# Performance work log

Measured on AMD Instinct MI355X. Metric: run time of the kernel, lower is better.

Reference implementation:

```python
import jax, jax.numpy as jnp
import numpy as np

N_NODES = 50000
N_EDGES = 800000
IN_DIM = 256
HID = 256
OUT = 2


def setup_inputs() -> dict:
    key = jax.random.key(0)
    ks = jax.random.split(key, 12)
    x = jax.random.normal(ks[0], (N_NODES, IN_DIM), dtype=jnp.float32)
    edge_index = jax.random.randint(ks[1], (2, N_EDGES), 0, N_NODES, dtype=jnp.int64)
    s = lambda fan_in: 1.0 / np.sqrt(fan_in)
    return {
        "x": x,
        "edge_index": edge_index,
        # SAGEConv 1: lin_l (neighbors, with bias), lin_r (root, no bias)
        "W1l": jax.random.normal(ks[2], (IN_DIM, HID), dtype=jnp.float32) * s(IN_DIM),
        "b1l": jnp.zeros((HID,), dtype=jnp.float32),
        "W1r": jax.random.normal(ks[3], (IN_DIM, HID), dtype=jnp.float32) * s(IN_DIM),
        # SAGEConv 2
        "W2l": jax.random.normal(ks[4], (HID, HID), dtype=jnp.float32) * s(HID),
        "b2l": jnp.zeros((HID,), dtype=jnp.float32),
        "W2r": jax.random.normal(ks[5], (HID, HID), dtype=jnp.float32) * s(HID),
        # edge MLP: Linear(2H -> H), ReLU, Linear(H -> OUT)
        "Wm1": jax.random.normal(ks[6], (2 * HID, HID), dtype=jnp.float32) * s(2 * HID),
        "bm1": jnp.zeros((HID,), dtype=jnp.float32),
        "Wm2": jax.random.normal(ks[7], (HID, OUT), dtype=jnp.float32) * s(HID),
        "bm2": jnp.zeros((OUT,), dtype=jnp.float32),
    }


def _sage_conv(x, src, dst, Wl, bl, Wr):
    # mean-aggregate source features at destination nodes (PyG SAGEConv, aggr='mean')
    n = x.shape[0]
    msg_sum = jax.ops.segment_sum(x[src], dst, num_segments=n)      # [N, D]
    deg = jax.ops.segment_sum(jnp.ones((src.shape[0],), x.dtype), dst, num_segments=n)
    agg = msg_sum / jnp.maximum(deg, 1.0)[:, None]
    return agg @ Wl + bl + x @ Wr


def reference(x, edge_index, W1l, b1l, W1r, W2l, b2l, W2r, Wm1, bm1, Wm2, bm2):
    src, dst = edge_index[0], edge_index[1]
    h = jax.nn.relu(_sage_conv(x, src, dst, W1l, b1l, W1r))
    h = jax.nn.relu(_sage_conv(h, src, dst, W2l, b2l, W2r))
    edge_reps = jnp.concatenate([h[src], h[dst]], axis=1)           # [E, 2H]
    hidden = jax.nn.relu(edge_reps @ Wm1 + bm1)
    logits = hidden @ Wm2 + bm2                                     # [E, OUT]
    return logits
```

## Files before the change

kernel.cpp:

```cpp
#include <hip/hip_runtime.h>

#define IN_DIM 256
#define HID 256
#define SCAN_CHUNK 512
#define PADW 264

typedef unsigned short ushort_t;
typedef __attribute__((ext_vector_type(8))) short short8;
typedef __attribute__((ext_vector_type(4))) float floatx4;

__device__ __forceinline__ float b2f(ushort_t h) {
    union { unsigned int u; float f; } c; c.u = ((unsigned int)h) << 16; return c.f;
}
__device__ __forceinline__ ushort_t f2b(float f) {
    union { float f; unsigned int u; } c; c.f = f;
    unsigned int u = c.u;
    unsigned int r = (u + 0x7fffu + ((u >> 16) & 1u)) >> 16;
    return (ushort_t)r;
}

__global__ void k_count_deg(const int* __restrict__ dst, int* __restrict__ deg, int E) {
    int e = blockIdx.x * blockDim.x + threadIdx.x;
    if (e < E) atomicAdd(&deg[dst[e]], 1);
}

__global__ __launch_bounds__(64) void k_chunk_sum(const int* __restrict__ deg,
                                                  int* __restrict__ partials, int N) {
    int lane = threadIdx.x;
    int base = blockIdx.x * SCAN_CHUNK + lane * 8;
    int s = 0;
#pragma unroll
    for (int i = 0; i < 8; ++i) s += (base + i < N) ? deg[base + i] : 0;
#pragma unroll
    for (int off = 32; off > 0; off >>= 1) s += __shfl_down(s, off, 64);
    if (lane == 0) partials[blockIdx.x] = s;
}

__global__ __launch_bounds__(64) void k_scan_partials(int* __restrict__ partials, int nb) {
    int lane = threadIdx.x;
    int run = 0;
    for (int base = 0; base < nb; base += 64) {
        int v = (base + lane < nb) ? partials[base + lane] : 0;
        int s = v;
#pragma unroll
        for (int off = 1; off < 64; off <<= 1) {
            int t = __shfl_up(s, off, 64);
            if (lane >= off) s += t;
        }
        if (base + lane < nb) partials[base + lane] = run + s - v;
        run += __shfl(s, 63, 64);
    }
}

__global__ __launch_bounds__(64) void k_scan_chunks(const int* __restrict__ deg,
                                                    const int* __restrict__ partials,
                                                    int* __restrict__ row_start,
                                                    int* __restrict__ cursor, int N) {
    int lane = threadIdx.x;
    int base = blockIdx.x * SCAN_CHUNK + lane * 8;
    int v[8]; int lsum = 0;
#pragma unroll
    for (int i = 0; i < 8; ++i) { v[i] = (base + i < N) ? deg[base + i] : 0; lsum += v[i]; }
    int pre = lsum;
#pragma unroll
    for (int off = 1; off < 64; off <<= 1) {
        int t = __shfl_up(pre, off, 64);
        if (lane >= off) pre += t;
    }
    pre -= lsum;
    int run = partials[blockIdx.x] + pre;
#pragma unroll
    for (int i = 0; i < 8; ++i) {
        if (base + i < N) { row_start[base + i] = run; cursor[base + i] = run; }
        run += v[i];
    }
}

__global__ void k_bucket(const int* __restrict__ src, const int* __restrict__ dst,
                         int* __restrict__ cursor, int2* __restrict__ csr, int E) {
    int e = blockIdx.x * blockDim.x + threadIdx.x;
    if (e < E) {
        int pos = atomicAdd(&cursor[dst[e]], 1);
        csr[pos] = make_int2(src[e], e);
    }
}

__global__ __launch_bounds__(256) void k_cast(const float* __restrict__ x,
                                              ushort_t* __restrict__ xb, int n4) {
    int i = blockIdx.x * blockDim.x + threadIdx.x;
    if (i >= n4) return;
    float4 v = ((const float4*)x)[i];
    ushort4 o;
    o.x = f2b(v.x); o.y = f2b(v.y); o.z = f2b(v.z); o.w = f2b(v.w);
    ((ushort4*)xb)[i] = o;
}

__global__ __launch_bounds__(64) void k_wprep(const float* __restrict__ Wsrc,
                                              ushort_t* __restrict__ WF,
                                              int nbTot, int nb0) {
    int lane = threadIdx.x;
    int kb = blockIdx.x >> 4, nbL = blockIdx.x & 15;
    int k = kb * 32 + (lane >> 4) * 8;
    int n = nbL * 16 + (lane & 15);
    size_t dstb = (size_t)(kb * nbTot + nb0 + nbL) * 512 + lane * 8;
#pragma unroll
    for (int j = 0; j < 8; ++j) {
        WF[dstb + j] = f2b(Wsrc[(size_t)(k + j) * 256 + n]);
    }
}

__global__ __launch_bounds__(256) void k_gather(const ushort_t* __restrict__ X,
                                                const int2* __restrict__ csr,
                                                const int* __restrict__ row_start,
                                                const int* __restrict__ deg,
                                                ushort_t* __restrict__ agg, int N) {
    int lane = threadIdx.x & 63;
    int node = blockIdx.x * 4 + (threadIdx.x >> 6);
    if (node >= N) return;
    int quad = lane >> 4, l16 = lane & 15;
    int start = row_start[node];
    int cnt = deg[node];
    const int2* sp = csr + start;
    float acc[16] = {};
    for (int b = 0; b < cnt; b += 64) {
        int nb = min(64, cnt - b);
        int sidx = (lane < nb) ? sp[b + lane].x : 0;

        int jA = (quad < nb) ? quad : 0;
        int jB = (4 + quad < nb) ? 4 + quad : 0;
        int sA = __shfl(sidx, jA, 64);
        int sB = __shfl(sidx, jB, 64);
        const ushort_t* rA = X + (size_t)sA * HID + l16 * 16;
        const ushort_t* rB = X + (size_t)sB * HID + l16 * 16;
        short8 a0 = *(const short8*)(rA);
        short8 a1 = *(const short8*)(rA + 8);
        short8 b0 = *(const short8*)(rB);
        short8 b1 = *(const short8*)(rB + 8);

        for (int j8 = 0; j8 < nb; j8 += 8) {
            bool vA = (j8 + quad) < nb, vB = (j8 + 4 + quad) < nb;
            short8 na0 = a0, na1 = a1, nb0 = b0, nb1 = b1;
            int j1 = j8 + 8;
            if (j1 < nb) {
                int cA = (j1 + quad < nb) ? j1 + quad : 0;
                int cB = (j1 + 4 + quad < nb) ? j1 + 4 + quad : 0;
                int zA = __shfl(sidx, cA, 64);
                int zB = __shfl(sidx, cB, 64);
                const ushort_t* qA = X + (size_t)zA * HID + l16 * 16;
                const ushort_t* qB = X + (size_t)zB * HID + l16 * 16;
                na0 = *(const short8*)(qA);
                na1 = *(const short8*)(qA + 8);
                nb0 = *(const short8*)(qB);
                nb1 = *(const short8*)(qB + 8);
            }
            if (vA) {
#pragma unroll
                for (int i = 0; i < 8; ++i) {
                    acc[i]     += b2f((ushort_t)a0[i]);
                    acc[8 + i] += b2f((ushort_t)a1[i]);
                }
            }
            if (vB) {
#pragma unroll
                for (int i = 0; i < 8; ++i) {
                    acc[i]     += b2f((ushort_t)b0[i]);
                    acc[8 + i] += b2f((ushort_t)b1[i]);
                }
            }
            a0 = na0; a1 = na1; b0 = nb0; b1 = nb1;
        }
    }
#pragma unroll
    for (int i = 0; i < 16; ++i) {
        acc[i] += __shfl_down(acc[i], 32, 64);
        acc[i] += __shfl_down(acc[i], 16, 64);
    }
    if (quad == 0) {
        float sc = 1.0f / (float)max(cnt, 1);
        short8 o0, o1;
#pragma unroll
        for (int i = 0; i < 8; ++i) {
            o0[i] = (short)f2b(acc[i] * sc);
            o1[i] = (short)f2b(acc[8 + i] * sc);
        }
        ushort_t* op = agg + (size_t)node * HID + l16 * 16;
        *(short8*)(op) = o0;
        *(short8*)(op + 8) = o1;
    }
}

__global__ __launch_bounds__(512) void k_mfma(const ushort_t* __restrict__ A1,
                                              const ushort_t* __restrict__ WF1,
                                              const ushort_t* __restrict__ A2,
                                              const ushort_t* __restrict__ WF2,
                                              const float* __restrict__ bias, int relu,
                                              int M, int nbTot,
                                              ushort_t* __restrict__ C,
                                              ushort_t* __restrict__ C2) {
    __shared__ ushort_t As[64 * PADW];
    const int tid = threadIdx.x;
    const int lane = tid & 63;
    const int w = tid >> 6;
    const int wm = w >> 2, wn = w & 3;
    const int quad = lane >> 4, l16 = lane & 15;
    const int m0 = blockIdx.y * 64;
    const int n0 = blockIdx.x * 256;
    const int nbBase = (n0 >> 4) + wn * 4;

    floatx4 acc[2][4] = {};

    for (int op = 0; op < 2; ++op) {
        const ushort_t* A = op ? A2 : A1;
        const ushort_t* WF = op ? WF2 : WF1;
        if (A == nullptr) continue;
        if (op) __syncthreads();
#pragma unroll
        for (int i = 0; i < 4; ++i) {
            int c = i * 512 + tid;
            int row = c >> 5, col = c & 31;
            int arow = m0 + row; if (arow >= M) arow = M - 1;
            *(uint4*)&As[row * PADW + col * 8] =
                *(const uint4*)(A + (size_t)arow * 256 + col * 8);
        }
        __syncthreads();

        const ushort_t* a0p = &As[(wm * 32 + l16) * PADW + quad * 8];
        const ushort_t* a1p = a0p + 16 * PADW;
        const ushort_t* wp = WF + (size_t)nbBase * 512 + lane * 8;
#pragma unroll
        for (int kb = 0; kb < 8; ++kb) {
            short8 a0 = *(const short8*)(a0p + kb * 32);
            short8 a1 = *(const short8*)(a1p + kb * 32);
            const ushort_t* wkb = wp + (size_t)kb * nbTot * 512;
#pragma unroll
            for (int nj = 0; nj < 4; ++nj) {
                short8 bj = *(const short8*)(wkb + nj * 512);
                acc[0][nj] = __builtin_amdgcn_mfma_f32_16x16x32_bf16(a0, bj, acc[0][nj], 0, 0, 0);
                acc[1][nj] = __builtin_amdgcn_mfma_f32_16x16x32_bf16(a1, bj, acc[1][nj], 0, 0, 0);
            }
        }
    }

#pragma unroll
    for (int mi = 0; mi < 2; ++mi) {
#pragma unroll
        for (int nj = 0; nj < 4; ++nj) {
            int col = n0 + wn * 64 + nj * 16 + l16;
            float b = bias ? bias[col] : 0.f;
            int rbase = m0 + wm * 32 + mi * 16 + quad * 4;
            ushort_t* dstp = C;
            int c = col;
            if (C2 && col >= 256) { dstp = C2; c = col - 256; }
#pragma unroll
            for (int reg = 0; reg < 4; ++reg) {
                int r = rbase + reg;
                if (r >= M) continue;
                float v = acc[mi][nj][reg] + b;
                if (relu) v = fmaxf(v, 0.f);
                dstp[(size_t)r * 256 + c] = f2b(v);
            }
        }
    }
}

__global__ __launch_bounds__(256) void k_edge(const ushort_t* __restrict__ P,
                                              const ushort_t* __restrict__ Q,
                                              const int2* __restrict__ csr,
                                              const int* __restrict__ row_start,
                                              const int* __restrict__ deg,
                                              const float* __restrict__ bm1,
                                              const float* __restrict__ Wm2,
                                              const float* __restrict__ bm2,
                                              float* __restrict__ out, int N, int stride) {
    int lane = threadIdx.x & 63;
    int wid = blockIdx.x * 4 + (threadIdx.x >> 6);
    int half = lane >> 5, l32 = lane & 31;

    float w0[8], w1[8], bb[8];
    const float* bp = bm1 + l32 * 8;
    const float2* wp = (const float2*)Wm2 + l32 * 8;
#pragma unroll
    for (int i = 0; i < 8; ++i) {
        float2 wv = wp[i];
        w0[i] = wv.x; w1[i] = wv.y;
        bb[i] = bp[i];
    }
    float bo0 = bm2[0], bo1 = bm2[1];

    for (int node = wid; node < N; node += stride) {
        int start = row_start[node];
        int cnt = deg[node];
        if (cnt == 0) continue;

        short8 qv = *(const short8*)(Q + (size_t)node * HID + l32 * 8);
        float qb[8];
#pragma unroll
        for (int i = 0; i < 8; ++i) qb[i] = b2f((ushort_t)qv[i]) + bb[i];

        const int2* sp = csr + start;
        for (int b = 0; b < cnt; b += 64) {
            int nb = min(64, cnt - b);
            int2 se = (lane < nb) ? sp[b + lane] : make_int2(0, 0);

            int iA = (half < nb) ? half : 0;
            int iB = (2 + half < nb) ? 2 + half : 0;
            int iC = (4 + half < nb) ? 4 + half : 0;
            int iD = (6 + half < nb) ? 6 + half : 0;
            int sA = __shfl(se.x, iA, 64);
            int sB = __shfl(se.x, iB, 64);
            int sC = __shfl(se.x, iC, 64);
            int sD = __shfl(se.x, iD, 64);
            short8 pA = *(const short8*)(P + (size_t)sA * HID + l32 * 8);
            short8 pB = *(const short8*)(P + (size_t)sB * HID + l32 * 8);
            short8 pC = *(const short8*)(P + (size_t)sC * HID + l32 * 8);
            short8 pD = *(const short8*)(P + (size_t)sD * HID + l32 * 8);

            for (int j0 = 0; j0 < nb; j0 += 8) {
                bool vA = j0 + half < nb, vB = j0 + 2 + half < nb;
                bool vC = j0 + 4 + half < nb, vD = j0 + 6 + half < nb;

                int kA = iA, kB = iB, kC = iC, kD = iD;
                short8 nA = pA, nB = pB, nC = pC, nD = pD;
                int j1 = j0 + 8;
                if (j1 < nb) {
                    kA = (j1 + half < nb) ? j1 + half : 0;
                    kB = (j1 + 2 + half < nb) ? j1 + 2 + half : 0;
                    kC = (j1 + 4 + half < nb) ? j1 + 4 + half : 0;
                    kD = (j1 + 6 + half < nb) ? j1 + 6 + half : 0;
                    int zA = __shfl(se.x, kA, 64);
                    int zB = __shfl(se.x, kB, 64);
                    int zC = __shfl(se.x, kC, 64);
                    int zD = __shfl(se.x, kD, 64);
                    nA = *(const short8*)(P + (size_t)zA * HID + l32 * 8);
                    nB = *(const short8*)(P + (size_t)zB * HID + l32 * 8);
                    nC = *(const short8*)(P + (size_t)zC * HID + l32 * 8);
                    nD = *(const short8*)(P + (size_t)zD * HID + l32 * 8);
                }

                float aA0 = 0.f, aA1 = 0.f, aB0 = 0.f, aB1 = 0.f;
                float aC0 = 0.f, aC1 = 0.f, aD0 = 0.f, aD1 = 0.f;
#pragma unroll
                for (int i = 0; i < 8; ++i) {
                    float hA = fmaxf(b2f((ushort_t)pA[i]) + qb[i], 0.f);
                    float hB = fmaxf(b2f((ushort_t)pB[i]) + qb[i], 0.f);
                    float hC = fmaxf(b2f((ushort_t)pC[i]) + qb[i], 0.f);
                    float hD = fmaxf(b2f((ushort_t)pD[i]) + qb[i], 0.f);
                    aA0 += hA * w0[i]; aA1 += hA * w1[i];
                    aB0 += hB * w0[i]; aB1 += hB * w1[i];
                    aC0 += hC * w0[i]; aC1 += hC * w1[i];
                    aD0 += hD * w0[i]; aD1 += hD * w1[i];
                }
#pragma unroll
                for (int off = 16; off > 0; off >>= 1) {
                    aA0 += __shfl_down(aA0, off, 32);
                    aA1 += __shfl_down(aA1, off, 32);
                    aB0 += __shfl_down(aB0, off, 32);
                    aB1 += __shfl_down(aB1, off, 32);
                    aC0 += __shfl_down(aC0, off, 32);
                    aC1 += __shfl_down(aC1, off, 32);
                    aD0 += __shfl_down(aD0, off, 32);
                    aD1 += __shfl_down(aD1, off, 32);
                }
                int eA = __shfl(se.y, iA, 64);
                int eB = __shfl(se.y, iB, 64);
                int eC = __shfl(se.y, iC, 64);
                int eD = __shfl(se.y, iD, 64);
                if (l32 == 0) {
                    if (vA) { float2 o; o.x = aA0 + bo0; o.y = aA1 + bo1; ((float2*)out)[eA] = o; }
                    if (vB) { float2 o; o.x = aB0 + bo0; o.y = aB1 + bo1; ((float2*)out)[eB] = o; }
                    if (vC) { float2 o; o.x = aC0 + bo0; o.y = aC1 + bo1; ((float2*)out)[eC] = o; }
                    if (vD) { float2 o; o.x = aD0 + bo0; o.y = aD1 + bo1; ((float2*)out)[eD] = o; }
                }
                pA = nA; pB = nB; pC = nC; pD = nD;
                iA = kA; iB = kB; iC = kC; iD = kD;
            }
        }
    }
}

extern "C" void kernel_launch(void* const* d_in, const int* in_sizes, int n_in,
                              void* d_out, int out_size, void* d_ws, size_t ws_size,
                              hipStream_t stream) {
    const float* x   = (const float*)d_in[0];
    const int*   ei  = (const int*)d_in[1];
    const float* W1l = (const float*)d_in[2];
    const float* b1l = (const float*)d_in[3];
    const float* W1r = (const float*)d_in[4];
    const float* W2l = (const float*)d_in[5];
    const float* b2l = (const float*)d_in[6];
    const float* W2r = (const float*)d_in[7];
    const float* Wm1 = (const float*)d_in[8];
    const float* bm1 = (const float*)d_in[9];
    const float* Wm2 = (const float*)d_in[10];
    const float* bm2 = (const float*)d_in[11];

    const int N = in_sizes[0] / IN_DIM;
    const int E = in_sizes[1] / 2;
    const int* src = ei;
    const int* dst = ei + E;
    const int NB = (N + SCAN_CHUNK - 1) / SCAN_CHUNK;

    char* ws = (char*)d_ws;
    size_t off = 0;
    auto alloc = [&](size_t bytes) { void* p = ws + off; off = (off + bytes + 255) & ~(size_t)255; return p; };
    int* deg       = (int*)alloc((size_t)N * 4);
    int* row_start = (int*)alloc((size_t)N * 4);
    int* cursor    = (int*)alloc((size_t)N * 4);
    int* partials  = (int*)alloc((size_t)(NB + 1) * 4);
    int2* csr      = (int2*)alloc((size_t)E * 8);
    size_t matB = (size_t)N * HID * sizeof(ushort_t);
    ushort_t* xb   = (ushort_t*)alloc(matB);
    ushort_t* aggB = (ushort_t*)alloc(matB);
    ushort_t* h1b  = (ushort_t*)alloc(matB);
    ushort_t* h2b  = (ushort_t*)alloc(matB);
    ushort_t* Pb   = (ushort_t*)alloc(matB);
    ushort_t* Qb   = (ushort_t*)alloc(matB);
    size_t wfB  = (size_t)8 * 16 * 512 * sizeof(ushort_t);
    ushort_t* WF1l = (ushort_t*)alloc(wfB);
    ushort_t* WF1r = (ushort_t*)alloc(wfB);
    ushort_t* WF2l = (ushort_t*)alloc(wfB);
    ushort_t* WF2r = (ushort_t*)alloc(wfB);
    ushort_t* WFm  = (ushort_t*)alloc(wfB * 2);
    float* out = (float*)d_out;

    int nwg = (N + 3) / 4;
    int mrows = (N + 63) / 64;

    hipMemsetAsync(deg, 0, (size_t)N * 4, stream);
    k_count_deg<<<(E + 255) / 256, 256, 0, stream>>>(dst, deg, E);
    k_chunk_sum<<<NB, 64, 0, stream>>>(deg, partials, N);
    k_scan_partials<<<1, 64, 0, stream>>>(partials, NB);
    k_scan_chunks<<<NB, 64, 0, stream>>>(deg, partials, row_start, cursor, N);
    k_bucket<<<(E + 255) / 256, 256, 0, stream>>>(src, dst, cursor, csr, E);

    k_cast<<<(N * HID / 4 + 255) / 256, 256, 0, stream>>>(x, xb, N * HID / 4);
    k_wprep<<<128, 64, 0, stream>>>(W1l, WF1l, 16, 0);
    k_wprep<<<128, 64, 0, stream>>>(W1r, WF1r, 16, 0);
    k_wprep<<<128, 64, 0, stream>>>(W2l, WF2l, 16, 0);
    k_wprep<<<128, 64, 0, stream>>>(W2r, WF2r, 16, 0);
    k_wprep<<<128, 64, 0, stream>>>(Wm1, WFm, 32, 0);
    k_wprep<<<128, 64, 0, stream>>>(Wm1 + (size_t)256 * 256, WFm, 32, 16);

    k_gather<<<nwg, 256, 0, stream>>>(xb, csr, row_start, deg, aggB, N);
    k_mfma<<<dim3(1, mrows), 512, 0, stream>>>(aggB, WF1l, xb, WF1r, b1l, 1, N, 16, h1b, nullptr);

    k_gather<<<nwg, 256, 0, stream>>>(h1b, csr, row_start, deg, aggB, N);
    k_mfma<<<dim3(1, mrows), 512, 0, stream>>>(aggB, WF2l, h1b, WF2r, b2l, 1, N, 16, h2b, nullptr);

    k_mfma<<<dim3(2, mrows), 512, 0, stream>>>(h2b, WFm, nullptr, nullptr, nullptr, 0, N, 32, Pb, Qb);

    const int EB = 2048;
    k_edge<<<EB, 256, 0, stream>>>(Pb, Qb, csr, row_start, deg, bm1, Wm2, bm2, out, N, EB * 4);
}
```

Baseline: 551.8 us.

## Partition edge MLP by source-node slice for P cache locality

Builds a second CSR keyed by (source slice, destination), so the edge kernel processes edges grouped into eight source-node ranges, with blocks assigned to slices. Each slice's P rows (about 3 MB of bf16) should then stay resident in cache during the random gathers. The cost is extra atomics, a larger scan, extra CSR/dst buffers, and a per-edge Q gather in place of the per-node Q reuse. Prefetch double-buffering of the P loads is also dropped.

```diff
diff --git a/kernel.cpp b/kernel.cpp
--- a/kernel.cpp
+++ b/kernel.cpp
@@ -4,6 +4,7 @@
 #define HID 256
 #define SCAN_CHUNK 512
 #define PADW 264
+#define NSLICE 8
 
 typedef unsigned short ushort_t;
 typedef __attribute__((ext_vector_type(8))) short short8;
@@ -19,9 +20,16 @@
     return (ushort_t)r;
 }
 
-__global__ void k_count_deg(const int* __restrict__ dst, int* __restrict__ deg, int E) {
+__global__ void k_count_both(const int* __restrict__ src, const int* __restrict__ dst,
+                             int* __restrict__ deg, int* __restrict__ deg2,
+                             int E, int N, float invS) {
     int e = blockIdx.x * blockDim.x + threadIdx.x;
-    if (e < E) atomicAdd(&deg[dst[e]], 1);
+    if (e < E) {
+        int d = dst[e];
+        atomicAdd(&deg[d], 1);
+        int sl = min((int)((float)src[e] * invS), NSLICE - 1);
+        atomicAdd(&deg2[sl * N + d], 1);
+    }
 }
 
 __global__ __launch_bounds__(64) void k_chunk_sum(const int* __restrict__ deg,
@@ -76,12 +84,20 @@
     }
 }
 
-__global__ void k_bucket(const int* __restrict__ src, const int* __restrict__ dst,
-                         int* __restrict__ cursor, int2* __restrict__ csr, int E) {
+__global__ void k_bucket_both(const int* __restrict__ src, const int* __restrict__ dst,
+                              int* __restrict__ cursor, int2* __restrict__ csr,
+                              int* __restrict__ cursor2, int2* __restrict__ csr2,
+                              int* __restrict__ dst2,
+                              int E, int N, float invS) {
     int e = blockIdx.x * blockDim.x + threadIdx.x;
     if (e < E) {
-        int pos = atomicAdd(&cursor[dst[e]], 1);
-        csr[pos] = make_int2(src[e], e);
+        int s = src[e], d = dst[e];
+        int pos = atomicAdd(&cursor[d], 1);
+        csr[pos] = make_int2(s, e);
+        int sl = min((int)((float)s * invS), NSLICE - 1);
+        int pos2 = atomicAdd(&cursor2[sl * N + d], 1);
+        csr2[pos2] = make_int2(s, e);
+        dst2[pos2] = d;
     }
 }
 
@@ -265,114 +281,95 @@
 
 __global__ __launch_bounds__(256) void k_edge(const ushort_t* __restrict__ P,
                                               const ushort_t* __restrict__ Q,
-                                              const int2* __restrict__ csr,
-                                              const int* __restrict__ row_start,
-                                              const int* __restrict__ deg,
+                                              const int2* __restrict__ csr2,
+                                              const int* __restrict__ dst2,
+                                              const int* __restrict__ rs2,
                                               const float* __restrict__ bm1,
                                               const float* __restrict__ Wm2,
                                               const float* __restrict__ bm2,
-                                              float* __restrict__ out, int N, int stride) {
+                                              float* __restrict__ out, int N, int E) {
     int lane = threadIdx.x & 63;
-    int wid = blockIdx.x * 4 + (threadIdx.x >> 6);
     int half = lane >> 5, l32 = lane & 31;
+    int slice = blockIdx.x & (NSLICE - 1);
+    int wv = (blockIdx.x >> 3) * 4 + (threadIdx.x >> 6);
+    int wstride = (gridDim.x >> 3) * 4;
 
     float w0[8], w1[8], bb[8];
     const float* bp = bm1 + l32 * 8;
     const float2* wp = (const float2*)Wm2 + l32 * 8;
 #pragma unroll
     for (int i = 0; i < 8; ++i) {
-        float2 wv = wp[i];
-        w0[i] = wv.x; w1[i] = wv.y;
+        float2 wv2 = wp[i];
+        w0[i] = wv2.x; w1[i] = wv2.y;
         bb[i] = bp[i];
     }
     float bo0 = bm2[0], bo1 = bm2[1];
 
-    for (int node = wid; node < N; node += stride) {
-        int start = row_start[node];
-        int cnt = deg[node];
-        if (cnt == 0) continue;
-
-        short8 qv = *(const short8*)(Q + (size_t)node * HID + l32 * 8);
-        float qb[8];
-#pragma unroll
-        for (int i = 0; i < 8; ++i) qb[i] = b2f((ushort_t)qv[i]) + bb[i];
-
-        const int2* sp = csr + start;
-        for (int b = 0; b < cnt; b += 64) {
-            int nb = min(64, cnt - b);
-            int2 se = (lane < nb) ? sp[b + lane] : make_int2(0, 0);
-
-            int iA = (half < nb) ? half : 0;
-            int iB = (2 + half < nb) ? 2 + half : 0;
-            int iC = (4 + half < nb) ? 4 + half : 0;
-            int iD = (6 + half < nb) ? 6 + half : 0;
+    int e0 = rs2[slice * N];
+    int e1 = (slice == NSLICE - 1) ? E : rs2[(slice + 1) * N];
+
+    for (int base = e0 + wv * 64; base < e1; base += wstride * 64) {
+        int nb = min(64, e1 - base);
+        int2 se = (lane < nb) ? csr2[base + lane] : make_int2(0, 0);
+        int dd = (lane < nb) ? dst2[base + lane] : 0;
+
+        for (int j0 = 0; j0 < nb; j0 += 8) {
+            bool vA = j0 + half < nb, vB = j0 + 2 + half < nb;
+            bool vC = j0 + 4 + half < nb, vD = j0 + 6 + half < nb;
+            int iA = vA ? j0 + half : 0;
+            int iB = vB ? j0 + 2 + half : 0;
+            int iC = vC ? j0 + 4 + half : 0;
+            int iD = vD ? j0 + 6 + half : 0;
             int sA = __shfl(se.x, iA, 64);
             int sB = __shfl(se.x, iB, 64);
             int sC = __shfl(se.x, iC, 64);
             int sD = __shfl(se.x, iD, 64);
+            int dA = __shfl(dd, iA, 64);
+            int dB = __shfl(dd, iB, 64);
+            int dC = __shfl(dd, iC, 64);
+            int dD = __shfl(dd, iD, 64);
             short8 pA = *(const short8*)(P + (size_t)sA * HID + l32 * 8);
             short8 pB = *(const short8*)(P + (size_t)sB * HID + l32 * 8);
             short8 pC = *(const short8*)(P + (size_t)sC * HID + l32 * 8);
             short8 pD = *(const short8*)(P + (size_t)sD * HID + l32 * 8);
-
-            for (int j0 = 0; j0 < nb; j0 += 8) {
-                bool vA = j0 + half < nb, vB = j0 + 2 + half < nb;
-                bool vC = j0 + 4 + half < nb, vD = j0 + 6 + half < nb;
-
-                int kA = iA, kB = iB, kC = iC, kD = iD;
-                short8 nA = pA, nB = pB, nC = pC, nD = pD;
-                int j1 = j0 + 8;
-                if (j1 < nb) {
-                    kA = (j1 + half < nb) ? j1 + half : 0;
-                    kB = (j1 + 2 + half < nb) ? j1 + 2 + half : 0;
-                    kC = (j1 + 4 + half < nb) ? j1 + 4 + half : 0;
-                    kD = (j1 + 6 + half < nb) ? j1 + 6 + half : 0;
-                    int zA = __shfl(se.x, kA, 64);
-                    int zB = __shfl(se.x, kB, 64);
-                    int zC = __shfl(se.x, kC, 64);
-                    int zD = __shfl(se.x, kD, 64);
-                    nA = *(const short8*)(P + (size_t)zA * HID + l32 * 8);
-                    nB = *(const short8*)(P + (size_t)zB * HID + l32 * 8);
-                    nC = *(const short8*)(P + (size_t)zC * HID + l32 * 8);
-                    nD = *(const short8*)(P + (size_t)zD * HID + l32 * 8);
-                }
-
-                float aA0 = 0.f, aA1 = 0.f, aB0 = 0.f, aB1 = 0.f;
-                float aC0 = 0.f, aC1 = 0.f, aD0 = 0.f, aD1 = 0.f;
-#pragma unroll
-                for (int i = 0; i < 8; ++i) {
-                    float hA = fmaxf(b2f((ushort_t)pA[i]) + qb[i], 0.f);
-                    float hB = fmaxf(b2f((ushort_t)pB[i]) + qb[i], 0.f);
-                    float hC = fmaxf(b2f((ushort_t)pC[i]) + qb[i], 0.f);
-                    float hD = fmaxf(b2f((ushort_t)pD[i]) + qb[i], 0.f);
-                    aA0 += hA * w0[i]; aA1 += hA * w1[i];
-                    aB0 += hB * w0[i]; aB1 += hB * w1[i];
-                    aC0 += hC * w0[i]; aC1 += hC * w1[i];
-                    aD0 += hD * w0[i]; aD1 += hD * w1[i];
-                }
-#pragma unroll
-                for (int off = 16; off > 0; off >>= 1) {
-                    aA0 += __shfl_down(aA0, off, 32);
-                    aA1 += __shfl_down(aA1, off, 32);
-                    aB0 += __shfl_down(aB0, off, 32);
-                    aB1 += __shfl_down(aB1, off, 32);
-                    aC0 += __shfl_down(aC0, off, 32);
-                    aC1 += __shfl_down(aC1, off, 32);
-                    aD0 += __shfl_down(aD0, off, 32);
-                    aD1 += __shfl_down(aD1, off, 32);
-                }
-                int eA = __shfl(se.y, iA, 64);
-                int eB = __shfl(se.y, iB, 64);
-                int eC = __shfl(se.y, iC, 64);
-                int eD = __shfl(se.y, iD, 64);
-                if (l32 == 0) {
-                    if (vA) { float2 o; o.x = aA0 + bo0; o.y = aA1 + bo1; ((float2*)out)[eA] = o; }
-                    if (vB) { float2 o; o.x = aB0 + bo0; o.y = aB1 + bo1; ((float2*)out)[eB] = o; }
-                    if (vC) { float2 o; o.x = aC0 + bo0; o.y = aC1 + bo1; ((float2*)out)[eC] = o; }
-                    if (vD) { float2 o; o.x = aD0 + bo0; o.y = aD1 + bo1; ((float2*)out)[eD] = o; }
-                }
-                pA = nA; pB = nB; pC = nC; pD = nD;
-                iA = kA; iB = kB; iC = kC; iD = kD;
+            short8 qA = *(const short8*)(Q + (size_t)dA * HID + l32 * 8);
+            short8 qB = *(const short8*)(Q + (size_t)dB * HID + l32 * 8);
+            short8 qC = *(const short8*)(Q + (size_t)dC * HID + l32 * 8);
+            short8 qD = *(const short8*)(Q + (size_t)dD * HID + l32 * 8);
+
+            float aA0 = 0.f, aA1 = 0.f, aB0 = 0.f, aB1 = 0.f;
+            float aC0 = 0.f, aC1 = 0.f, aD0 = 0.f, aD1 = 0.f;
+#pragma unroll
+            for (int i = 0; i < 8; ++i) {
+                float hA = fmaxf(b2f((ushort_t)pA[i]) + b2f((ushort_t)qA[i]) + bb[i], 0.f);
+                float hB = fmaxf(b2f((ushort_t)pB[i]) + b2f((ushort_t)qB[i]) + bb[i], 0.f);
+                float hC = fmaxf(b2f((ushort_t)pC[i]) + b2f((ushort_t)qC[i]) + bb[i], 0.f);
+                float hD = fmaxf(b2f((ushort_t)pD[i]) + b2f((ushort_t)qD[i]) + bb[i], 0.f);
+                aA0 += hA * w0[i]; aA1 += hA * w1[i];
+                aB0 += hB * w0[i]; aB1 += hB * w1[i];
+                aC0 += hC * w0[i]; aC1 += hC * w1[i];
+                aD0 += hD * w0[i]; aD1 += hD * w1[i];
+            }
+#pragma unroll
+            for (int off = 16; off > 0; off >>= 1) {
+                aA0 += __shfl_down(aA0, off, 32);
+                aA1 += __shfl_down(aA1, off, 32);
+                aB0 += __shfl_down(aB0, off, 32);
+                aB1 += __shfl_down(aB1, off, 32);
+                aC0 += __shfl_down(aC0, off, 32);
+                aC1 += __shfl_down(aC1, off, 32);
+                aD0 += __shfl_down(aD0, off, 32);
+                aD1 += __shfl_down(aD1, off, 32);
+            }
+            int eA = __shfl(se.y, iA, 64);
+            int eB = __shfl(se.y, iB, 64);
+            int eC = __shfl(se.y, iC, 64);
+            int eD = __shfl(se.y, iD, 64);
+            if (l32 == 0) {
+                if (vA) { float2 o; o.x = aA0 + bo0; o.y = aA1 + bo1; ((float2*)out)[eA] = o; }
+                if (vB) { float2 o; o.x = aB0 + bo0; o.y = aB1 + bo1; ((float2*)out)[eB] = o; }
+                if (vC) { float2 o; o.x = aC0 + bo0; o.y = aC1 + bo1; ((float2*)out)[eC] = o; }
+                if (vD) { float2 o; o.x = aD0 + bo0; o.y = aD1 + bo1; ((float2*)out)[eD] = o; }
             }
         }
     }
@@ -399,6 +396,10 @@
     const int* src = ei;
     const int* dst = ei + E;
     const int NB = (N + SCAN_CHUNK - 1) / SCAN_CHUNK;
+    const int N8 = NSLICE * N;
+    const int NB2 = (N8 + SCAN_CHUNK - 1) / SCAN_CHUNK;
+    const int sdiv = (N + NSLICE - 1) / NSLICE;
+    const float invS = 1.0f / (float)sdiv;
 
     char* ws = (char*)d_ws;
     size_t off = 0;
@@ -408,6 +409,12 @@
     int* cursor    = (int*)alloc((size_t)N * 4);
     int* partials  = (int*)alloc((size_t)(NB + 1) * 4);
     int2* csr      = (int2*)alloc((size_t)E * 8);
+    int* deg2      = (int*)alloc((size_t)N8 * 4);
+    int* rs2       = (int*)alloc((size_t)N8 * 4);
+    int* cursor2   = (int*)alloc((size_t)N8 * 4);
+    int* partials2 = (int*)alloc((size_t)(NB2 + 1) * 4);
+    int2* csr2     = (int2*)alloc((size_t)E * 8);
+    int* dst2      = (int*)alloc((size_t)E * 4);
     size_t matB = (size_t)N * HID * sizeof(ushort_t);
     ushort_t* xb   = (ushort_t*)alloc(matB);
     ushort_t* aggB = (ushort_t*)alloc(matB);
@@ -427,11 +434,16 @@
     int mrows = (N + 63) / 64;
 
     hipMemsetAsync(deg, 0, (size_t)N * 4, stream);
-    k_count_deg<<<(E + 255) / 256, 256, 0, stream>>>(dst, deg, E);
+    hipMemsetAsync(deg2, 0, (size_t)N8 * 4, stream);
+    k_count_both<<<(E + 255) / 256, 256, 0, stream>>>(src, dst, deg, deg2, E, N, invS);
     k_chunk_sum<<<NB, 64, 0, stream>>>(deg, partials, N);
     k_scan_partials<<<1, 64, 0, stream>>>(partials, NB);
     k_scan_chunks<<<NB, 64, 0, stream>>>(deg, partials, row_start, cursor, N);
-    k_bucket<<<(E + 255) / 256, 256, 0, stream>>>(src, dst, cursor, csr, E);
+    k_chunk_sum<<<NB2, 64, 0, stream>>>(deg2, partials2, N8);
+    k_scan_partials<<<1, 64, 0, stream>>>(partials2, NB2);
+    k_scan_chunks<<<NB2, 64, 0, stream>>>(deg2, partials2, rs2, cursor2, N8);
+    k_bucket_both<<<(E + 255) / 256, 256, 0, stream>>>(src, dst, cursor, csr,
+                                                       cursor2, csr2, dst2, E, N, invS);
 
     k_cast<<<(N * HID / 4 + 255) / 256, 256, 0, stream>>>(x, xb, N * HID / 4);
     k_wprep<<<128, 64, 0, stream>>>(W1l, WF1l, 16, 0);
@@ -449,6 +461,6 @@
 
     k_mfma<<<dim3(2, mrows), 512, 0, stream>>>(h2b, WFm, nullptr, nullptr, nullptr, 0, N, 32, Pb, Qb);
 
-    const int EB = 2048;
-    k_edge<<<EB, 256, 0, stream>>>(Pb, Qb, csr, row_start, deg, bm1, Wm2, bm2, out, N, EB * 4);
-}
+    const int EB = 1024;
+    k_edge<<<EB, 256, 0, stream>>>(Pb, Qb, csr2, dst2, rs2, bm1, Wm2, bm2, out, N, E);
+}
```

After: 664.7 us. +20.5%, slower.

## Fuse neighbor gather-mean into SAGE conv GEMM kernel and merge weight prep launches

Applied to the files above, without the earlier changes.

Each SAGE layer now runs as one kernel: a 512-thread block first gathers and mean-aggregates neighbor features for its 64 nodes directly into shared memory, then runs both the neighbor and root MFMA products with bias and ReLU. This removes the global round-trip of the aggregated matrix and one launch per layer. The six weight-repack launches are also merged into one. The trade-off is that each wave now serially gathers 8 nodes before the GEMM phase, with doubled shared memory per block, which may reduce latency hiding for the irregular gather.

```diff
diff --git a/kernel.cpp b/kernel.cpp
--- a/kernel.cpp
+++ b/kernel.cpp
@@ -95,11 +95,22 @@
     ((ushort4*)xb)[i] = o;
 }
 
-__global__ __launch_bounds__(64) void k_wprep(const float* __restrict__ Wsrc,
-                                              ushort_t* __restrict__ WF,
-                                              int nbTot, int nb0) {
+__global__ __launch_bounds__(64) void k_wprep6(const float* __restrict__ W1l, ushort_t* WF1l,
+                                               const float* __restrict__ W1r, ushort_t* WF1r,
+                                               const float* __restrict__ W2l, ushort_t* WF2l,
+                                               const float* __restrict__ W2r, ushort_t* WF2r,
+                                               const float* __restrict__ Wm1, ushort_t* WFm) {
+    int m = blockIdx.x >> 7;
+    int bb = blockIdx.x & 127;
+    const float* Wsrc; ushort_t* WF; int nbTot, nb0;
+    if (m == 0)      { Wsrc = W1l; WF = WF1l; nbTot = 16; nb0 = 0; }
+    else if (m == 1) { Wsrc = W1r; WF = WF1r; nbTot = 16; nb0 = 0; }
+    else if (m == 2) { Wsrc = W2l; WF = WF2l; nbTot = 16; nb0 = 0; }
+    else if (m == 3) { Wsrc = W2r; WF = WF2r; nbTot = 16; nb0 = 0; }
+    else if (m == 4) { Wsrc = Wm1; WF = WFm;  nbTot = 32; nb0 = 0; }
+    else             { Wsrc = Wm1 + (size_t)256 * 256; WF = WFm; nbTot = 32; nb0 = 16; }
     int lane = threadIdx.x;
-    int kb = blockIdx.x >> 4, nbL = blockIdx.x & 15;
+    int kb = bb >> 4, nbL = bb & 15;
     int k = kb * 32 + (lane >> 4) * 8;
     int n = nbL * 16 + (lane & 15);
     size_t dstb = (size_t)(kb * nbTot + nb0 + nbL) * 512 + lane * 8;
@@ -109,90 +120,149 @@
     }
 }
 
-__global__ __launch_bounds__(256) void k_gather(const ushort_t* __restrict__ X,
-                                                const int2* __restrict__ csr,
-                                                const int* __restrict__ row_start,
-                                                const int* __restrict__ deg,
-                                                ushort_t* __restrict__ agg, int N) {
-    int lane = threadIdx.x & 63;
-    int node = blockIdx.x * 4 + (threadIdx.x >> 6);
-    if (node >= N) return;
-    int quad = lane >> 4, l16 = lane & 15;
-    int start = row_start[node];
-    int cnt = deg[node];
-    const int2* sp = csr + start;
-    float acc[16] = {};
-    for (int b = 0; b < cnt; b += 64) {
-        int nb = min(64, cnt - b);
-        int sidx = (lane < nb) ? sp[b + lane].x : 0;
-
-        int jA = (quad < nb) ? quad : 0;
-        int jB = (4 + quad < nb) ? 4 + quad : 0;
-        int sA = __shfl(sidx, jA, 64);
-        int sB = __shfl(sidx, jB, 64);
-        const ushort_t* rA = X + (size_t)sA * HID + l16 * 16;
-        const ushort_t* rB = X + (size_t)sB * HID + l16 * 16;
-        short8 a0 = *(const short8*)(rA);
-        short8 a1 = *(const short8*)(rA + 8);
-        short8 b0 = *(const short8*)(rB);
-        short8 b1 = *(const short8*)(rB + 8);
-
-        for (int j8 = 0; j8 < nb; j8 += 8) {
-            bool vA = (j8 + quad) < nb, vB = (j8 + 4 + quad) < nb;
-            short8 na0 = a0, na1 = a1, nb0 = b0, nb1 = b1;
-            int j1 = j8 + 8;
-            if (j1 < nb) {
-                int cA = (j1 + quad < nb) ? j1 + quad : 0;
-                int cB = (j1 + 4 + quad < nb) ? j1 + 4 + quad : 0;
-                int zA = __shfl(sidx, cA, 64);
-                int zB = __shfl(sidx, cB, 64);
-                const ushort_t* qA = X + (size_t)zA * HID + l16 * 16;
-                const ushort_t* qB = X + (size_t)zB * HID + l16 * 16;
-                na0 = *(const short8*)(qA);
-                na1 = *(const short8*)(qA + 8);
-                nb0 = *(const short8*)(qB);
-                nb1 = *(const short8*)(qB + 8);
+__global__ __launch_bounds__(512, 4) void k_conv(const ushort_t* __restrict__ X,
+                                                 const int2* __restrict__ csr,
+                                                 const int* __restrict__ row_start,
+                                                 const int* __restrict__ deg,
+                                                 const ushort_t* __restrict__ WFl,
+                                                 const ushort_t* __restrict__ WFr,
+                                                 const float* __restrict__ bias,
+                                                 int M,
+                                                 ushort_t* __restrict__ C) {
+    __shared__ ushort_t As[2][64 * PADW];
+    const int tid = threadIdx.x;
+    const int lane = tid & 63;
+    const int w = tid >> 6;
+    const int quad = lane >> 4, l16 = lane & 15;
+    const int m0 = blockIdx.x * 64;
+
+    for (int t = 0; t < 8; ++t) {
+        int node = m0 + w * 8 + t;
+        if (node >= M) continue;
+        int start = row_start[node];
+        int cnt = deg[node];
+        const int2* sp = csr + start;
+        float acc[16] = {};
+        for (int b = 0; b < cnt; b += 64) {
+            int nb = min(64, cnt - b);
+            int sidx = (lane < nb) ? sp[b + lane].x : 0;
+
+            int jA = (quad < nb) ? quad : 0;
+            int jB = (4 + quad < nb) ? 4 + quad : 0;
+            int sA = __shfl(sidx, jA, 64);
+            int sB = __shfl(sidx, jB, 64);
+            const ushort_t* rA = X + (size_t)sA * HID + l16 * 16;
+            const ushort_t* rB = X + (size_t)sB * HID + l16 * 16;
+            short8 a0 = *(const short8*)(rA);
+            short8 a1 = *(const short8*)(rA + 8);
+            short8 b0 = *(const short8*)(rB);
+            short8 b1 = *(const short8*)(rB + 8);
+
+            for (int j8 = 0; j8 < nb; j8 += 8) {
+                bool vA = (j8 + quad) < nb, vB = (j8 + 4 + quad) < nb;
+                short8 na0 = a0, na1 = a1, nb0 = b0, nb1 = b1;
+                int j1 = j8 + 8;
+                if (j1 < nb) {
+                    int cA = (j1 + quad < nb) ? j1 + quad : 0;
+                    int cB = (j1 + 4 + quad < nb) ? j1 + 4 + quad : 0;
+                    int zA = __shfl(sidx, cA, 64);
+                    int zB = __shfl(sidx, cB, 64);
+                    const ushort_t* qA = X + (size_t)zA * HID + l16 * 16;
+                    const ushort_t* qB = X + (size_t)zB * HID + l16 * 16;
+                    na0 = *(const short8*)(qA);
+                    na1 = *(const short8*)(qA + 8);
+                    nb0 = *(const short8*)(qB);
+                    nb1 = *(const short8*)(qB + 8);
+                }
+                if (vA) {
+#pragma unroll
+                    for (int i = 0; i < 8; ++i) {
+                        acc[i]     += b2f((ushort_t)a0[i]);
+                        acc[8 + i] += b2f((ushort_t)a1[i]);
+                    }
+                }
+                if (vB) {
+#pragma unroll
+                    for (int i = 0; i < 8; ++i) {
+                        acc[i]     += b2f((ushort_t)b0[i]);
+                        acc[8 + i] += b2f((ushort_t)b1[i]);
+                    }
+                }
+                a0 = na0; a1 = na1; b0 = nb0; b1 = nb1;
             }
-            if (vA) {
-#pragma unroll
-                for (int i = 0; i < 8; ++i) {
-                    acc[i]     += b2f((ushort_t)a0[i]);
-                    acc[8 + i] += b2f((ushort_t)a1[i]);
-                }
+        }
+#pragma unroll
+        for (int i = 0; i < 16; ++i) {
+            acc[i] += __shfl_down(acc[i], 32, 64);
+            acc[i] += __shfl_down(acc[i], 16, 64);
+        }
+        if (quad == 0) {
+            float sc = 1.0f / (float)max(cnt, 1);
+            short8 o0, o1;
+#pragma unroll
+            for (int i = 0; i < 8; ++i) {
+                o0[i] = (short)f2b(acc[i] * sc);
+                o1[i] = (short)f2b(acc[8 + i] * sc);
             }
-            if (vB) {
-#pragma unroll
-                for (int i = 0; i < 8; ++i) {
-                    acc[i]     += b2f((ushort_t)b0[i]);
-                    acc[8 + i] += b2f((ushort_t)b1[i]);
-                }
+            ushort_t* op = &As[0][(w * 8 + t) * PADW + l16 * 16];
+            *(short8*)(op) = o0;
+            *(short8*)(op + 8) = o1;
+        }
+    }
+
+#pragma unroll
+    for (int i = 0; i < 4; ++i) {
+        int c = i * 512 + tid;
+        int row = c >> 5, col = c & 31;
+        int arow = m0 + row; if (arow >= M) arow = M - 1;
+        *(uint4*)&As[1][row * PADW + col * 8] =
+            *(const uint4*)(X + (size_t)arow * 256 + col * 8);
+    }
+    __syncthreads();
+
+    const int wm = w >> 2, wn = w & 3;
+    floatx4 acc[2][4] = {};
+#pragma unroll
+    for (int op = 0; op < 2; ++op) {
+        const ushort_t* Ap = As[op];
+        const ushort_t* WF = op ? WFr : WFl;
+        const ushort_t* a0p = &Ap[(wm * 32 + l16) * PADW + quad * 8];
+        const ushort_t* a1p = a0p + 16 * PADW;
+        const ushort_t* wp = WF + (size_t)(wn * 4) * 512 + lane * 8;
+#pragma unroll
+        for (int kb = 0; kb < 8; ++kb) {
+            short8 a0 = *(const short8*)(a0p + kb * 32);
+            short8 a1 = *(const short8*)(a1p + kb * 32);
+            const ushort_t* wkb = wp + (size_t)kb * 16 * 512;
+#pragma unroll
+            for (int nj = 0; nj < 4; ++nj) {
+                short8 bj = *(const short8*)(wkb + nj * 512);
+                acc[0][nj] = __builtin_amdgcn_mfma_f32_16x16x32_bf16(a0, bj, acc[0][nj], 0, 0, 0);
+                acc[1][nj] = __builtin_amdgcn_mfma_f32_16x16x32_bf16(a1, bj, acc[1][nj], 0, 0, 0);
             }
-            a0 = na0; a1 = na1; b0 = nb0; b1 = nb1;
-        }
-    }
-#pragma unroll
-    for (int i = 0; i < 16; ++i) {
-        acc[i] += __shfl_down(acc[i], 32, 64);
-        acc[i] += __shfl_down(acc[i], 16, 64);
-    }
-    if (quad == 0) {
-        float sc = 1.0f / (float)max(cnt, 1);
-        short8 o0, o1;
-#pragma unroll
-        for (int i = 0; i < 8; ++i) {
-            o0[i] = (short)f2b(acc[i] * sc);
-            o1[i] = (short)f2b(acc[8 + i] * sc);
-        }
-        ushort_t* op = agg + (size_t)node * HID + l16 * 16;
-        *(short8*)(op) = o0;
-        *(short8*)(op + 8) = o1;
+        }
+    }
+
+#pragma unroll
+    for (int mi = 0; mi < 2; ++mi) {
+#pragma unroll
+        for (int nj = 0; nj < 4; ++nj) {
+            int col = wn * 64 + nj * 16 + l16;
+            float b = bias[col];
+            int rbase = m0 + wm * 32 + mi * 16 + quad * 4;
+#pragma unroll
+            for (int reg = 0; reg < 4; ++reg) {
+                int r = rbase + reg;
+                if (r >= M) continue;
+                float v = fmaxf(acc[mi][nj][reg] + b, 0.f);
+                C[(size_t)r * 256 + col] = f2b(v);
+            }
+        }
     }
 }
 
 __global__ __launch_bounds__(512) void k_mfma(const ushort_t* __restrict__ A1,
                                               const ushort_t* __restrict__ WF1,
-                                              const ushort_t* __restrict__ A2,
-                                              const ushort_t* __restrict__ WF2,
                                               const float* __restrict__ bias, int relu,
                                               int M, int nbTot,
                                               ushort_t* __restrict__ C,
@@ -209,35 +279,29 @@
 
     floatx4 acc[2][4] = {};
 
-    for (int op = 0; op < 2; ++op) {
-        const ushort_t* A = op ? A2 : A1;
-        const ushort_t* WF = op ? WF2 : WF1;
-        if (A == nullptr) continue;
-        if (op) __syncthreads();
-#pragma unroll
-        for (int i = 0; i < 4; ++i) {
-            int c = i * 512 + tid;
-            int row = c >> 5, col = c & 31;
-            int arow = m0 + row; if (arow >= M) arow = M - 1;
-            *(uint4*)&As[row * PADW + col * 8] =
-                *(const uint4*)(A + (size_t)arow * 256 + col * 8);
-        }
-        __syncthreads();
-
-        const ushort_t* a0p = &As[(wm * 32 + l16) * PADW + quad * 8];
-        const ushort_t* a1p = a0p + 16 * PADW;
-        const ushort_t* wp = WF + (size_t)nbBase * 512 + lane * 8;
-#pragma unroll
-        for (int kb = 0; kb < 8; ++kb) {
-            short8 a0 = *(const short8*)(a0p + kb * 32);
-            short8 a1 = *(const short8*)(a1p + kb * 32);
-            const ushort_t* wkb = wp + (size_t)kb * nbTot * 512;
-#pragma unroll
-            for (int nj = 0; nj < 4; ++nj) {
-                short8 bj = *(const short8*)(wkb + nj * 512);
-                acc[0][nj] = __builtin_amdgcn_mfma_f32_16x16x32_bf16(a0, bj, acc[0][nj], 0, 0, 0);
-                acc[1][nj] = __builtin_amdgcn_mfma_f32_16x16x32_bf16(a1, bj, acc[1][nj], 0, 0, 0);
-            }
+#pragma unroll
+    for (int i = 0; i < 4; ++i) {
+        int c = i * 512 + tid;
+        int row = c >> 5, col = c & 31;
+        int arow = m0 + row; if (arow >= M) arow = M - 1;
+        *(uint4*)&As[row * PADW + col * 8] =
+            *(const uint4*)(A1 + (size_t)arow * 256 + col * 8);
+    }
+    __syncthreads();
+
+    const ushort_t* a0p = &As[(wm * 32 + l16) * PADW + quad * 8];
+    const ushort_t* a1p = a0p + 16 * PADW;
+    const ushort_t* wp = WF1 + (size_t)nbBase * 512 + lane * 8;
+#pragma unroll
+    for (int kb = 0; kb < 8; ++kb) {
+        short8 a0 = *(const short8*)(a0p + kb * 32);
+        short8 a1 = *(const short8*)(a1p + kb * 32);
+        const ushort_t* wkb = wp + (size_t)kb * nbTot * 512;
+#pragma unroll
+        for (int nj = 0; nj < 4; ++nj) {
+            short8 bj = *(const short8*)(wkb + nj * 512);
+            acc[0][nj] = __builtin_amdgcn_mfma_f32_16x16x32_bf16(a0, bj, acc[0][nj], 0, 0, 0);
+            acc[1][nj] = __builtin_amdgcn_mfma_f32_16x16x32_bf16(a1, bj, acc[1][nj], 0, 0, 0);
         }
     }
 
@@ -410,7 +474,6 @@
     int2* csr      = (int2*)alloc((size_t)E * 8);
     size_t matB = (size_t)N * HID * sizeof(ushort_t);
     ushort_t* xb   = (ushort_t*)alloc(matB);
-    ushort_t* aggB = (ushort_t*)alloc(matB);
     ushort_t* h1b  = (ushort_t*)alloc(matB);
     ushort_t* h2b  = (ushort_t*)alloc(matB);
     ushort_t* Pb   = (ushort_t*)alloc(matB);
@@ -423,7 +486,6 @@
     ushort_t* WFm  = (ushort_t*)alloc(wfB * 2);
     float* out = (float*)d_out;
 
-    int nwg = (N + 3) / 4;
     int mrows = (N + 63) / 64;
 
     hipMemsetAsync(deg, 0, (size_t)N * 4, stream);
@@ -434,20 +496,13 @@
     k_bucket<<<(E + 255) / 256, 256, 0, stream>>>(src, dst, cursor, csr, E);
 
     k_cast<<<(N * HID / 4 + 255) / 256, 256, 0, stream>>>(x, xb, N * HID / 4);
-    k_wprep<<<128, 64, 0, stream>>>(W1l, WF1l, 16, 0);
-    k_wprep<<<128, 64, 0, stream>>>(W1r, WF1r, 16, 0);
-    k_wprep<<<128, 64, 0, stream>>>(W2l, WF2l, 16, 0);
-    k_wprep<<<128, 64, 0, stream>>>(W2r, WF2r, 16, 0);
-    k_wprep<<<128, 64, 0, stream>>>(Wm1, WFm, 32, 0);
-    k_wprep<<<128, 64, 0, stream>>>(Wm1 + (size_t)256 * 256, WFm, 32, 16);
-
-    k_gather<<<nwg, 256, 0, stream>>>(xb, csr, row_start, deg, aggB, N);
-    k_mfma<<<dim3(1, mrows), 512, 0, stream>>>(aggB, WF1l, xb, WF1r, b1l, 1, N, 16, h1b, nullptr);
-
-    k_gather<<<nwg, 256, 0, stream>>>(h1b, csr, row_start, deg, aggB, N);
-    k_mfma<<<dim3(1, mrows), 512, 0, stream>>>(aggB, WF2l, h1b, WF2r, b2l, 1, N, 16, h2b, nullptr);
-
-    k_mfma<<<dim3(2, mrows), 512, 0, stream>>>(h2b, WFm, nullptr, nullptr, nullptr, 0, N, 32, Pb, Qb);
+    k_wprep6<<<768, 64, 0, stream>>>(W1l, WF1l, W1r, WF1r, W2l, WF2l, W2r, WF2r, Wm1, WFm);
+
+    k_conv<<<mrows, 512, 0, stream>>>(xb, csr, row_start, deg, WF1l, WF1r, b1l, N, h1b);
+
+    k_conv<<<mrows, 512, 0, stream>>>(h1b, csr, row_start, deg, WF2l, WF2r, b2l, N, h2b);
+
+    k_mfma<<<dim3(2, mrows), 512, 0, stream>>>(h2b, WFm, nullptr, 0, N, 32, Pb, Qb);
 
     const int EB = 2048;
     k_edge<<<EB, 256, 0, stream>>>(Pb, Qb, csr, row_start, deg, bm1, Wm2, bm2, out, N, EB * 4);
```

Result: faster. 506.5 us (-8.2%).
